# Optimization experiments

Hardware: AMD Instinct MI355X
Metric: run time of the kernel (lower is better)

The kernel has to match this reference:

```python
import math
import jax, jax.numpy as jnp
import numpy as np

INPUT_DIM = 512
HIDDEN_DIM = 512
BATCH = 8
SEQ_LEN = 4096


def _xavier(key, shape):
    fan_out, fan_in = shape
    limit = math.sqrt(6.0 / (fan_in + fan_out))
    return jax.random.uniform(key, shape, jnp.float32, -limit, limit)


def setup_inputs() -> dict:
    key = jax.random.key(0)
    kx, kA, kB, kC, kD, kWg = jax.random.split(key, 6)
    return {
        "x": jax.random.normal(kx, (BATCH, SEQ_LEN, INPUT_DIM), jnp.float32),
        "A": jax.random.uniform(kA, (HIDDEN_DIM,), jnp.float32, 0.8, 0.95),
        "B": _xavier(kB, (HIDDEN_DIM, INPUT_DIM)),
        "C": _xavier(kC, (HIDDEN_DIM, HIDDEN_DIM)),
        "D": _xavier(kD, (HIDDEN_DIM, INPUT_DIM)),
        "Wg": _xavier(kWg, (HIDDEN_DIM, INPUT_DIM)),
        "bias_h": jnp.zeros((HIDDEN_DIM,), jnp.float32),
        "bias_y": jnp.zeros((HIDDEN_DIM,), jnp.float32),
    }


def reference(x, A, B, C, D, Wg, bias_h, bias_y):
    # x: (b, t, i). Eval mode: dropout is identity.
    hidden_dim = A.shape[0]
    # Precompute all input-dependent per-step terms as batched GEMMs.
    g = jnp.clip(jax.nn.sigmoid(jnp.einsum('bti,hi->bth', x, Wg)), 0.05, 0.95)
    xB = jnp.einsum('bti,hi->bth', x, B)
    # h_t = h_{t-1} + g_t*(A*h_{t-1} + xB_t + bias_h - h_{t-1})
    #     = (1 - g_t*(1 - A)) * h_{t-1} + g_t*(xB_t + bias_h)
    a_coef = 1.0 - g * (1.0 - A)          # (b, t, h)
    b_coef = g * (xB + bias_h)            # (b, t, h)

    def step(h, ab):
        a_t, b_t = ab
        h = a_t * h + b_t
        return h, h

    h0 = jnp.zeros((x.shape[0], hidden_dim), x.dtype)
    _, hs = jax.lax.scan(step, h0, (jnp.swapaxes(a_coef, 0, 1), jnp.swapaxes(b_coef, 0, 1)))
    hs = jnp.swapaxes(hs, 0, 1)           # (b, t, h)

    scale = 1.0 / math.sqrt(hidden_dim)
    y = (jnp.einsum('bth,oh->bto', hs, C) + jnp.einsum('bti,hi->bth', x, D) + bias_y) * scale
    return y
```

## Files before the change

kernel.cpp:

```cpp
#include <hip/hip_runtime.h>
#include <math.h>

#define MTOT 32768
#define KD 512
#define HD 512
#define NB 8
#define TS 4096
#define NCHUNK 64
#define TCHUNK 64

typedef __attribute__((ext_vector_type(8))) short bf16x8;
typedef __attribute__((ext_vector_type(4))) float f32x4;
typedef __attribute__((ext_vector_type(4))) unsigned short us4;

#define GLD16(gsrc, ldst) __builtin_amdgcn_global_load_lds( \
    (const __attribute__((address_space(1))) void*)(gsrc),   \
    (__attribute__((address_space(3))) void*)(ldst), 16, 0, 0)

__device__ __forceinline__ unsigned short f2bf(float f) {
    unsigned u = __float_as_uint(f);
    return (unsigned short)((u + 0x7FFFu + ((u >> 16) & 1u)) >> 16);
}
__device__ __forceinline__ float bf2f(unsigned short u) {
    return __uint_as_float(((unsigned)u) << 16);
}

__global__ __launch_bounds__(256) void cast_all(
    const float* __restrict__ x, const float* __restrict__ B,
    const float* __restrict__ G, const float* __restrict__ C,
    const float* __restrict__ D,
    unsigned short* __restrict__ x16, unsigned short* __restrict__ w16)
{
    const int blk = blockIdx.x;
    const float* src;
    unsigned short* dst;
    int i;
    if (blk < (MTOT * KD / 1024)) {
        src = x; dst = x16;
        i = blk * 1024 + threadIdx.x * 4;
    } else {
        const int r = blk - (MTOT * KD / 1024);
        const int mat = r >> 8;
        src = (mat == 0) ? B : (mat == 1) ? G : (mat == 2) ? C : D;
        dst = w16 + (size_t)mat * (HD * KD);
        i = (r & 255) * 1024 + threadIdx.x * 4;
    }
    float4 v = *(const float4*)(src + i);
    us4 o; o.x = f2bf(v.x); o.y = f2bf(v.y); o.z = f2bf(v.z); o.w = f2bf(v.w);
    *(us4*)(dst + i) = o;
}

__global__ __launch_bounds__(256, 2) void in_gemm_mfma(
    const short* __restrict__ xb, const short* __restrict__ wmat,
    const float* __restrict__ Avec, const float* __restrict__ bias_h,
    unsigned* __restrict__ ab16, float2* __restrict__ chPS)
{
    __shared__ __align__(16) short Xs[2][128 * 64];
    __shared__ __align__(16) short Ws[2][2][64 * 64];
    const int tid = threadIdx.x;
    const int w = tid >> 6, l = tid & 63;
    const int bid = blockIdx.x;
    const int xcd = bid & 7;
    const int jj  = bid >> 3;
    const int n0  = (jj & 7) * 64;
    const int m0  = (xcd * 32 + (jj >> 3)) * 128;
    const int wm = (w & 1) * 64;
    const int wn = (w >> 1) * 32;

    int xsrc[4], xdst[4];
    #pragma unroll
    for (int j = 0; j < 4; ++j) {
        const int s = (w * 4 + j) * 64 + l;
        const int r = s >> 3, g = (s & 7) ^ (r & 7);
        xsrc[j] = (m0 + r) * KD + g * 8;
        xdst[j] = (w * 4 + j) * 64 * 8;
    }
    int wsrc[2], wdst[2];
    #pragma unroll
    for (int j = 0; j < 2; ++j) {
        const int s = (w * 2 + j) * 64 + l;
        const int r = s >> 3, g = (s & 7) ^ (r & 7);
        wsrc[j] = (n0 + r) * KD + g * 8;
        wdst[j] = (w * 2 + j) * 64 * 8;
    }

#define STAGE_IN(TI, BUF) do {                                              \
    const int kk_ = (TI) * 64;                                              \
    _Pragma("unroll")                                                       \
    for (int j_ = 0; j_ < 4; ++j_)                                          \
        GLD16(xb + xsrc[j_] + kk_, &Xs[BUF][xdst[j_]]);                     \
    _Pragma("unroll")                                                       \
    for (int m_ = 0; m_ < 2; ++m_)                                          \
        _Pragma("unroll")                                                   \
        for (int j_ = 0; j_ < 2; ++j_)                                      \
            GLD16(wmat + (size_t)m_ * (HD * KD) + wsrc[j_] + kk_,           \
                  &Ws[BUF][m_][wdst[j_]]);                                  \
} while (0)

    f32x4 acc[2][4][2];
    #pragma unroll
    for (int a = 0; a < 2; ++a)
        #pragma unroll
        for (int i = 0; i < 4; ++i)
            #pragma unroll
            for (int j = 0; j < 2; ++j) acc[a][i][j] = (f32x4)0.0f;

    STAGE_IN(0, 0);
    STAGE_IN(1, 1);

    #pragma unroll
    for (int it = 0; it < 8; ++it) {
        const int cur = it & 1;
        if (it < 7) asm volatile("s_waitcnt vmcnt(8)" ::: "memory");
        else        asm volatile("s_waitcnt vmcnt(0)" ::: "memory");
        __builtin_amdgcn_s_barrier();
        __builtin_amdgcn_s_setprio(1);
        #pragma unroll
        for (int kc = 0; kc < 2; ++kc) {
            const int g = kc * 4 + (l >> 4);
            bf16x8 af[4];
            #pragma unroll
            for (int mt = 0; mt < 4; ++mt) {
                const int r = wm + mt * 16 + (l & 15);
                af[mt] = *(const bf16x8*)(&Xs[cur][r * 64 + ((g ^ (r & 7)) * 8)]);
            }
            #pragma unroll
            for (int mat = 0; mat < 2; ++mat) {
                #pragma unroll
                for (int nt = 0; nt < 2; ++nt) {
                    const int r = wn + nt * 16 + (l & 15);
                    bf16x8 bfv = *(const bf16x8*)(&Ws[cur][mat][r * 64 + ((g ^ (r & 7)) * 8)]);
                    #pragma unroll
                    for (int mt = 0; mt < 4; ++mt)
                        acc[mat][mt][nt] = __builtin_amdgcn_mfma_f32_16x16x32_bf16(
                            af[mt], bfv, acc[mat][mt][nt], 0, 0, 0);
                }
            }
        }
        __builtin_amdgcn_s_setprio(0);
        asm volatile("s_waitcnt lgkmcnt(0)" ::: "memory");
        __builtin_amdgcn_s_barrier();
        if (it < 6) STAGE_IN(it + 2, cur);
    }
#undef STAGE_IN

    const int q  = l >> 4;
    const int cl = l & 15;
    const int bidx   = m0 >> 12;
    const int c_in_b = ((m0 & (TS - 1)) >> 6) + (w & 1);
    #pragma unroll
    for (int nt = 0; nt < 2; ++nt) {
        const int n = n0 + wn + nt * 16 + cl;
        const float An1 = 1.0f - Avec[n];
        const float bh  = bias_h[n];
        float Pc = 1.0f, Sc = 0.0f;
        #pragma unroll
        for (int mt = 0; mt < 4; ++mt) {
            float Pl = 1.0f, Sl = 0.0f;
            #pragma unroll
            for (int r = 0; r < 4; ++r) {
                const float vB = acc[0][mt][nt][r];
                const float vG = acc[1][mt][nt][r];
                float g = __builtin_amdgcn_rcpf(1.0f + __expf(-vG));
                g = fminf(fmaxf(g, 0.05f), 0.95f);
                const unsigned short su = f2bf(g * An1);
                const unsigned short bu = f2bf(g * (vB + bh));
                const float a  = 1.0f - bf2f(su);
                const float bb = bf2f(bu);
                const int m = m0 + wm + mt * 16 + q * 4 + r;
                ab16[(size_t)m * HD + n] = (unsigned)su | ((unsigned)bu << 16);
                Sl = fmaf(a, Sl, bb);
                Pl *= a;
            }
            float Pm = 1.0f, Sm = 0.0f;
            #pragma unroll
            for (int k = 0; k < 4; ++k) {
                const float Pk = __shfl(Pl, cl + 16 * k, 64);
                const float Sk = __shfl(Sl, cl + 16 * k, 64);
                Sm = fmaf(Pk, Sm, Sk);
                Pm *= Pk;
            }
            Sc = fmaf(Pm, Sc, Sm);
            Pc *= Pm;
        }
        if (q == 0) {
            chPS[(size_t)c_in_b * (NB * HD) + bidx * HD + n] = make_float2(Pc, Sc);
        }
    }
}

__global__ __launch_bounds__(256) void scan_pass3(
    const unsigned* __restrict__ ab, const float2* __restrict__ chPS,
    unsigned short* __restrict__ hs_out)
{
    const int g = blockIdx.x * blockDim.x + threadIdx.x;
    const int h4 = (g & 127) * 4;
    const int rest = g >> 7;
    const int b = rest & (NB - 1);
    const int c = rest >> 3;
    const float2* p = chPS + (size_t)b * HD + h4;
    float hv0 = 0.0f, hv1 = 0.0f, hv2 = 0.0f, hv3 = 0.0f;
    for (int jc = 0; jc < c; ++jc) {
        const float4 ps01 = *(const float4*)(p + (size_t)jc * (NB * HD));
        const float4 ps23 = *(const float4*)(p + (size_t)jc * (NB * HD) + 2);
        hv0 = fmaf(ps01.x, hv0, ps01.y);
        hv1 = fmaf(ps01.z, hv1, ps01.w);
        hv2 = fmaf(ps23.x, hv2, ps23.y);
        hv3 = fmaf(ps23.z, hv3, ps23.w);
    }
    size_t idx = ((size_t)(b * TS + c * TCHUNK)) * HD + h4;
    #pragma unroll 4
    for (int t = 0; t < TCHUNK; ++t) {
        const uint4 v = *(const uint4*)(ab + idx);
        const float a0 = 1.0f - bf2f((unsigned short)(v.x & 0xFFFFu));
        const float a1 = 1.0f - bf2f((unsigned short)(v.y & 0xFFFFu));
        const float a2 = 1.0f - bf2f((unsigned short)(v.z & 0xFFFFu));
        const float a3 = 1.0f - bf2f((unsigned short)(v.w & 0xFFFFu));
        hv0 = fmaf(a0, hv0, bf2f((unsigned short)(v.x >> 16)));
        hv1 = fmaf(a1, hv1, bf2f((unsigned short)(v.y >> 16)));
        hv2 = fmaf(a2, hv2, bf2f((unsigned short)(v.z >> 16)));
        hv3 = fmaf(a3, hv3, bf2f((unsigned short)(v.w >> 16)));
        us4 o; o.x = f2bf(hv0); o.y = f2bf(hv1); o.z = f2bf(hv2); o.w = f2bf(hv3);
        *(us4*)(hs_out + idx) = o;
        idx += HD;
    }
}

__global__ __launch_bounds__(256, 2) void out_gemm_dual(
    const short* __restrict__ hs, const short* __restrict__ xb,
    const short* __restrict__ Cb, const short* __restrict__ Db,
    const float* __restrict__ bias_y, float* __restrict__ y)
{
    __shared__ __align__(16) short Hs[128 * 64];
    __shared__ __align__(16) short Xs2[128 * 64];
    __shared__ __align__(16) short Cs[128 * 64];
    __shared__ __align__(16) short Ds[128 * 64];
    const int tid = threadIdx.x;
    const int w = tid >> 6, l = tid & 63;
    const int bid = blockIdx.x;
    const int xcd = bid & 7;
    const int jj  = bid >> 3;
    const int n0  = (jj & 3) * 128;
    const int m0  = (xcd * 32 + (jj >> 2)) * 128;
    const int wm = (w & 1) * 64;
    const int wn = (w >> 1) * 64;

    int src_m[4], src_n[4], dst_s[4];
    #pragma unroll
    for (int j = 0; j < 4; ++j) {
        const int s = (w * 4 + j) * 64 + l;
        const int r = s >> 3, g = (s & 7) ^ (r & 7);
        src_m[j] = (m0 + r) * HD + g * 8;
        src_n[j] = (n0 + r) * HD + g * 8;
        dst_s[j] = (w * 4 + j) * 64 * 8;
    }

    f32x4 acc[4][4];
    #pragma unroll
    for (int i = 0; i < 4; ++i)
        #pragma unroll
        for (int j = 0; j < 4; ++j) acc[i][j] = (f32x4)0.0f;

    for (int kk = 0; kk < HD; kk += 64) {
        __syncthreads();
        #pragma unroll
        for (int j = 0; j < 4; ++j) {
            GLD16(hs + src_m[j] + kk, Hs  + dst_s[j]);
            GLD16(xb + src_m[j] + kk, Xs2 + dst_s[j]);
            GLD16(Cb + src_n[j] + kk, Cs  + dst_s[j]);
            GLD16(Db + src_n[j] + kk, Ds  + dst_s[j]);
        }
        __syncthreads();
        #pragma unroll
        for (int kc = 0; kc < 2; ++kc) {
            const int g = kc * 4 + (l >> 4);
            {
                bf16x8 af[4], bfv[4];
                #pragma unroll
                for (int t = 0; t < 4; ++t) {
                    const int ra = wm + t * 16 + (l & 15);
                    af[t] = *(const bf16x8*)(Hs + ra * 64 + ((g ^ (ra & 7)) * 8));
                    const int rb = wn + t * 16 + (l & 15);
                    bfv[t] = *(const bf16x8*)(Cs + rb * 64 + ((g ^ (rb & 7)) * 8));
                }
                #pragma unroll
                for (int mt = 0; mt < 4; ++mt)
                    #pragma unroll
                    for (int nt = 0; nt < 4; ++nt)
                        acc[mt][nt] = __builtin_amdgcn_mfma_f32_16x16x32_bf16(
                            af[mt], bfv[nt], acc[mt][nt], 0, 0, 0);
            }
            {
                bf16x8 af[4], bfv[4];
                #pragma unroll
                for (int t = 0; t < 4; ++t) {
                    const int ra = wm + t * 16 + (l & 15);
                    af[t] = *(const bf16x8*)(Xs2 + ra * 64 + ((g ^ (ra & 7)) * 8));
                    const int rb = wn + t * 16 + (l & 15);
                    bfv[t] = *(const bf16x8*)(Ds + rb * 64 + ((g ^ (rb & 7)) * 8));
                }
                #pragma unroll
                for (int mt = 0; mt < 4; ++mt)
                    #pragma unroll
                    for (int nt = 0; nt < 4; ++nt)
                        acc[mt][nt] = __builtin_amdgcn_mfma_f32_16x16x32_bf16(
                            af[mt], bfv[nt], acc[mt][nt], 0, 0, 0);
            }
        }
    }

    const float scale = 0.04419417382415922f;
    #pragma unroll
    for (int nt = 0; nt < 4; ++nt) {
        const int n = n0 + wn + nt * 16 + (l & 15);
        const float by = bias_y[n];
        #pragma unroll
        for (int mt = 0; mt < 4; ++mt) {
            #pragma unroll
            for (int r = 0; r < 4; ++r) {
                const int m = m0 + wm + mt * 16 + (l >> 4) * 4 + r;
                y[(size_t)m * HD + n] = (acc[mt][nt][r] + by) * scale;
            }
        }
    }
}

extern "C" void kernel_launch(void* const* d_in, const int* in_sizes, int n_in,
                              void* d_out, int out_size, void* d_ws, size_t ws_size,
                              hipStream_t stream) {
    const float* x      = (const float*)d_in[0];
    const float* Avec   = (const float*)d_in[1];
    const float* Bw     = (const float*)d_in[2];
    const float* Cw     = (const float*)d_in[3];
    const float* Dw     = (const float*)d_in[4];
    const float* Wg     = (const float*)d_in[5];
    const float* bias_h = (const float*)d_in[6];
    const float* bias_y = (const float*)d_in[7];
    float* y = (float*)d_out;

    unsigned* ab16        = (unsigned*)d_ws;
    unsigned short* x16   = (unsigned short*)(ab16 + (size_t)MTOT * HD);
    unsigned short* hs16  = x16 + (size_t)MTOT * HD;
    unsigned short* w16   = hs16 + (size_t)MTOT * HD;
    float2* chPS = (float2*)(w16 + (size_t)4 * HD * KD);

    cast_all<<<MTOT * KD / 1024 + 4 * (HD * KD / 1024), 256, 0, stream>>>(
        x, Bw, Wg, Cw, Dw, x16, w16);

    in_gemm_mfma<<<2048, 256, 0, stream>>>(
        (const short*)x16, (const short*)w16, Avec, bias_h, ab16, chPS);

    scan_pass3<<<(NB * HD * NCHUNK / 4) / 256, 256, 0, stream>>>(ab16, chPS, hs16);

    out_gemm_dual<<<1024, 256, 0, stream>>>(
        (const short*)hs16, (const short*)x16,
        (const short*)(w16 + (size_t)2 * HD * KD),
        (const short*)(w16 + (size_t)3 * HD * KD), bias_y, y);
}
```

Measured before the change: 254.5 us.

## Halve in_gemm K-tile to raise occupancy; use plain 2D grid in out_gemm

The input GEMM now stages 32-wide K tiles instead of 64, with a new XOR swizzle and 16 pipeline iterations. This halves its LDS footprint so the launch bound can ask for 4 blocks per CU instead of 2. It also drops the XCD-aware block remapping in the output GEMM in favour of a simple 2D grid. The trade-off is more barriers and waitcnts per K step, register pressure at the higher occupancy target, and possibly worse L2 locality per XCD in the output GEMM.

Result: no change. 250.8 us (-1.5%).

```diff
diff --git a/kernel.cpp b/kernel.cpp
--- a/kernel.cpp
+++ b/kernel.cpp
@@ -50,13 +50,13 @@
     *(us4*)(dst + i) = o;
 }
 
-__global__ __launch_bounds__(256, 2) void in_gemm_mfma(
+__global__ __launch_bounds__(256, 4) void in_gemm_mfma(
     const short* __restrict__ xb, const short* __restrict__ wmat,
     const float* __restrict__ Avec, const float* __restrict__ bias_h,
     unsigned* __restrict__ ab16, float2* __restrict__ chPS)
 {
-    __shared__ __align__(16) short Xs[2][128 * 64];
-    __shared__ __align__(16) short Ws[2][2][64 * 64];
+    __shared__ __align__(16) short Xs[2][128 * 32];
+    __shared__ __align__(16) short Ws[2][2][64 * 32];
     const int tid = threadIdx.x;
     const int w = tid >> 6, l = tid & 63;
     const int bid = blockIdx.x;
@@ -67,34 +67,31 @@
     const int wm = (w & 1) * 64;
     const int wn = (w >> 1) * 32;
 
-    int xsrc[4], xdst[4];
-    #pragma unroll
-    for (int j = 0; j < 4; ++j) {
-        const int s = (w * 4 + j) * 64 + l;
-        const int r = s >> 3, g = (s & 7) ^ (r & 7);
-        xsrc[j] = (m0 + r) * KD + g * 8;
-        xdst[j] = (w * 4 + j) * 64 * 8;
-    }
-    int wsrc[2], wdst[2];
+    int xsrc[2], xdst[2];
     #pragma unroll
     for (int j = 0; j < 2; ++j) {
         const int s = (w * 2 + j) * 64 + l;
-        const int r = s >> 3, g = (s & 7) ^ (r & 7);
-        wsrc[j] = (n0 + r) * KD + g * 8;
-        wdst[j] = (w * 2 + j) * 64 * 8;
+        const int r = s >> 2, gg = (s & 3) ^ ((r >> 1) & 3);
+        xsrc[j] = (m0 + r) * KD + gg * 8;
+        xdst[j] = s * 8;
+    }
+    int wsrc, wdsts;
+    {
+        const int s = w * 64 + l;
+        const int r = s >> 2, gg = (s & 3) ^ ((r >> 1) & 3);
+        wsrc = (n0 + r) * KD + gg * 8;
+        wdsts = s * 8;
     }
 
 #define STAGE_IN(TI, BUF) do {                                              \
-    const int kk_ = (TI) * 64;                                              \
+    const int kk_ = (TI) * 32;                                              \
     _Pragma("unroll")                                                       \
-    for (int j_ = 0; j_ < 4; ++j_)                                          \
+    for (int j_ = 0; j_ < 2; ++j_)                                          \
         GLD16(xb + xsrc[j_] + kk_, &Xs[BUF][xdst[j_]]);                     \
     _Pragma("unroll")                                                       \
     for (int m_ = 0; m_ < 2; ++m_)                                          \
-        _Pragma("unroll")                                                   \
-        for (int j_ = 0; j_ < 2; ++j_)                                      \
-            GLD16(wmat + (size_t)m_ * (HD * KD) + wsrc[j_] + kk_,           \
-                  &Ws[BUF][m_][wdst[j_]]);                                  \
+        GLD16(wmat + (size_t)m_ * (HD * KD) + wsrc + kk_,                   \
+              &Ws[BUF][m_][wdsts]);                                         \
 } while (0)
 
     f32x4 acc[2][4][2];
@@ -108,39 +105,38 @@
     STAGE_IN(0, 0);
     STAGE_IN(1, 1);
 
-    #pragma unroll
-    for (int it = 0; it < 8; ++it) {
+    const int g = l >> 4;
+    #pragma unroll
+    for (int it = 0; it < 16; ++it) {
         const int cur = it & 1;
-        if (it < 7) asm volatile("s_waitcnt vmcnt(8)" ::: "memory");
-        else        asm volatile("s_waitcnt vmcnt(0)" ::: "memory");
+        if (it < 15) asm volatile("s_waitcnt vmcnt(4)" ::: "memory");
+        else         asm volatile("s_waitcnt vmcnt(0)" ::: "memory");
         __builtin_amdgcn_s_barrier();
         __builtin_amdgcn_s_setprio(1);
-        #pragma unroll
-        for (int kc = 0; kc < 2; ++kc) {
-            const int g = kc * 4 + (l >> 4);
-            bf16x8 af[4];
-            #pragma unroll
-            for (int mt = 0; mt < 4; ++mt) {
-                const int r = wm + mt * 16 + (l & 15);
-                af[mt] = *(const bf16x8*)(&Xs[cur][r * 64 + ((g ^ (r & 7)) * 8)]);
-            }
-            #pragma unroll
-            for (int mat = 0; mat < 2; ++mat) {
-                #pragma unroll
-                for (int nt = 0; nt < 2; ++nt) {
-                    const int r = wn + nt * 16 + (l & 15);
-                    bf16x8 bfv = *(const bf16x8*)(&Ws[cur][mat][r * 64 + ((g ^ (r & 7)) * 8)]);
-                    #pragma unroll
-                    for (int mt = 0; mt < 4; ++mt)
-                        acc[mat][mt][nt] = __builtin_amdgcn_mfma_f32_16x16x32_bf16(
-                            af[mt], bfv, acc[mat][mt][nt], 0, 0, 0);
-                }
+        bf16x8 af[4];
+        #pragma unroll
+        for (int mt = 0; mt < 4; ++mt) {
+            const int r = wm + mt * 16 + (l & 15);
+            const int sg = g ^ ((r >> 1) & 3);
+            af[mt] = *(const bf16x8*)(&Xs[cur][r * 32 + sg * 8]);
+        }
+        #pragma unroll
+        for (int mat = 0; mat < 2; ++mat) {
+            #pragma unroll
+            for (int nt = 0; nt < 2; ++nt) {
+                const int r = wn + nt * 16 + (l & 15);
+                const int sg = g ^ ((r >> 1) & 3);
+                bf16x8 bfv = *(const bf16x8*)(&Ws[cur][mat][r * 32 + sg * 8]);
+                #pragma unroll
+                for (int mt = 0; mt < 4; ++mt)
+                    acc[mat][mt][nt] = __builtin_amdgcn_mfma_f32_16x16x32_bf16(
+                        af[mt], bfv, acc[mat][mt][nt], 0, 0, 0);
             }
         }
         __builtin_amdgcn_s_setprio(0);
         asm volatile("s_waitcnt lgkmcnt(0)" ::: "memory");
         __builtin_amdgcn_s_barrier();
-        if (it < 6) STAGE_IN(it + 2, cur);
+        if (it < 14) STAGE_IN(it + 2, cur);
     }
 #undef STAGE_IN
 
@@ -161,10 +157,10 @@
             for (int r = 0; r < 4; ++r) {
                 const float vB = acc[0][mt][nt][r];
                 const float vG = acc[1][mt][nt][r];
-                float g = __builtin_amdgcn_rcpf(1.0f + __expf(-vG));
-                g = fminf(fmaxf(g, 0.05f), 0.95f);
-                const unsigned short su = f2bf(g * An1);
-                const unsigned short bu = f2bf(g * (vB + bh));
+                float g2 = __builtin_amdgcn_rcpf(1.0f + __expf(-vG));
+                g2 = fminf(fmaxf(g2, 0.05f), 0.95f);
+                const unsigned short su = f2bf(g2 * An1);
+                const unsigned short bu = f2bf(g2 * (vB + bh));
                 const float a  = 1.0f - bf2f(su);
                 const float bb = bf2f(bu);
                 const int m = m0 + wm + mt * 16 + q * 4 + r;
@@ -237,11 +233,8 @@
     __shared__ __align__(16) short Ds[128 * 64];
     const int tid = threadIdx.x;
     const int w = tid >> 6, l = tid & 63;
-    const int bid = blockIdx.x;
-    const int xcd = bid & 7;
-    const int jj  = bid >> 3;
-    const int n0  = (jj & 3) * 128;
-    const int m0  = (xcd * 32 + (jj >> 2)) * 128;
+    const int m0 = blockIdx.x * 128;
+    const int n0 = blockIdx.y * 128;
     const int wm = (w & 1) * 64;
     const int wn = (w >> 1) * 64;
 
@@ -352,7 +345,7 @@
 
     scan_pass3<<<(NB * HD * NCHUNK / 4) / 256, 256, 0, stream>>>(ab16, chPS, hs16);
 
-    out_gemm_dual<<<1024, 256, 0, stream>>>(
+    out_gemm_dual<<<dim3(MTOT / 128, HD / 128), 256, 0, stream>>>(
         (const short*)hs16, (const short*)x16,
         (const short*)(w16 + (size_t)2 * HD * KD),
         (const short*)(w16 + (size_t)3 * HD * KD), bias_y, y);
```
